# Performance work log

Measured on AMD Instinct MI355X. Metric: run time of the kernel, lower is better.

## Reference

```python
import jax, jax.numpy as jnp
import numpy as np

N_NODES = 100000


def setup_inputs() -> dict:
    key = jax.random.key(0)
    ks = jax.random.split(key, 7)
    n, d, c, e = N_NODES, 256, 128, 3200000
    features = jax.random.normal(ks[0], (n, d), dtype=jnp.float32)
    adj_row = jax.random.randint(ks[1], (e,), 0, n, dtype=jnp.int32)
    adj_col = jax.random.randint(ks[2], (e,), 0, n, dtype=jnp.int32)
    adj_vals = jax.random.uniform(ks[3], (e,), dtype=jnp.float32)
    kernel = jax.random.normal(ks[4], (d, c), dtype=jnp.float32) * (1.0 / np.sqrt(d))
    bias = jax.random.normal(ks[5], (c,), dtype=jnp.float32) * 0.01
    skip_weight = jax.random.normal(ks[6], (c,), dtype=jnp.float32)
    return {"features": features, "adj_row": adj_row, "adj_col": adj_col,
            "adj_vals": adj_vals, "kernel": kernel, "bias": bias,
            "skip_weight": skip_weight}


def reference(features, adj_row, adj_col, adj_vals, kernel, bias, skip_weight):
    # h = X @ W  : [n, c]
    h = features @ kernel
    # SpMM: out[r] += A[r, c] * h[c] over edges (COO)
    msgs = adj_vals[:, None] * h[adj_col]            # [e, c]
    agg = jax.ops.segment_sum(msgs, adj_row, num_segments=N_NODES)  # [n, c]
    out = h * skip_weight + agg                      # skip-connection scale + aggregation
    out = out + bias
    return jax.nn.selu(out)
```

## Files before the change

kernel.cpp:

```cpp
#include <hip/hip_runtime.h>
#include <math.h>

#define N_NODES 100000
#define D 256
#define C 128
#define N_EDGES 3200000

#define BROWS 128
#define NBUCKET ((N_NODES + BROWS - 1) / BROWS)
#define CAP 4608
#define EPB 8192
#define PBLOCKS ((N_EDGES + EPB - 1) / EPB)
#define NCH 13
#define NKEY (BROWS * NCH)

typedef __attribute__((ext_vector_type(8))) short bf16x8;
typedef __attribute__((ext_vector_type(4))) float f32x4;

__device__ __forceinline__ unsigned short f2bf(float f) {
  const unsigned int u = __float_as_uint(f);
  return (unsigned short)((u + 0x7fffu + ((u >> 16) & 1u)) >> 16);
}
__device__ __forceinline__ unsigned int pack_bf(float lo, float hi) {
  return (unsigned int)f2bf(lo) | ((unsigned int)f2bf(hi) << 16);
}
__device__ __forceinline__ float bflo(unsigned int u) {
  return __uint_as_float(u << 16);
}
__device__ __forceinline__ float bfhi(unsigned int u) {
  return __uint_as_float(u & 0xffff0000u);
}
__device__ __forceinline__ float selu1(float x) {
  const float scale = 1.0507009873554804934193349852946f;
  const float alpha = 1.6732632423543772848170429916717f;
  return x > 0.f ? scale * x : scale * alpha * (__expf(x) - 1.f);
}
__device__ __forceinline__ unsigned int pack_rec(int col, float val) {
  return ((unsigned int)col << 15) | ((unsigned int)f2bf(val) & 0x7fffu);
}
__device__ __forceinline__ float rec_val(unsigned int r) {
  return __uint_as_float((r & 0x7fffu) << 16);
}
__device__ __forceinline__ bf16x8 packA_nt(const float* p) {
  const f32x4 a0 = __builtin_nontemporal_load(reinterpret_cast<const f32x4*>(p));
  const f32x4 a1 =
      __builtin_nontemporal_load(reinterpret_cast<const f32x4*>(p) + 1);
  union {
    unsigned int u[4];
    bf16x8 v;
  } af;
  af.u[0] = pack_bf(a0[0], a0[1]);
  af.u[1] = pack_bf(a0[2], a0[3]);
  af.u[2] = pack_bf(a1[0], a1[1]);
  af.u[3] = pack_bf(a1[2], a1[3]);
  return af.v;
}

__global__ __launch_bounds__(256) void prep(const float* __restrict__ W,
                                            unsigned short* __restrict__ WT) {
  const int t = blockIdx.x * blockDim.x + threadIdx.x;
  const int n = t >> 8;
  const int k = t & 255;
  WT[t] = f2bf(W[k * C + n]);
}

__global__ __launch_bounds__(512) void gemm_partition(
    const float* __restrict__ X, const unsigned short* __restrict__ WT,
    unsigned short* __restrict__ h2, const int* __restrict__ row,
    const int* __restrict__ col, const float* __restrict__ vals,
    unsigned int* __restrict__ meta, uint2* __restrict__ recs) {
  __shared__ int hist[NBUCKET];
  __shared__ int scanA[1024];
  __shared__ int scanB[1024];
  const int bid = blockIdx.x;
  const int tid = threadIdx.x;

  if ((bid & 1) == 0) {
    const int wid = (bid >> 1) * 8 + (tid >> 6);
    const int row0 = wid * 32;
    if (row0 >= N_NODES) return;
    const int lane = tid & 63;
    const int r = lane & 15;
    const int kg = lane >> 4;

    f32x4 acc[2][8];
#pragma unroll
    for (int g = 0; g < 2; ++g)
#pragma unroll
      for (int f = 0; f < 8; ++f) acc[g][f] = (f32x4){0.f, 0.f, 0.f, 0.f};

    const float* arow0 = X + (size_t)(row0 + r) * D + kg * 8;
    const float* arow1 = arow0 + 16 * D;
    for (int k0 = 0; k0 < D; k0 += 32) {
      const bf16x8 a0 = packA_nt(arow0 + k0);
      const bf16x8 a1 = packA_nt(arow1 + k0);
#pragma unroll
      for (int f = 0; f < 8; ++f) {
        const bf16x8 bf = *reinterpret_cast<const bf16x8*>(
            WT + (size_t)(f * 16 + r) * D + k0 + kg * 8);
        acc[0][f] =
            __builtin_amdgcn_mfma_f32_16x16x32_bf16(a0, bf, acc[0][f], 0, 0, 0);
        acc[1][f] =
            __builtin_amdgcn_mfma_f32_16x16x32_bf16(a1, bf, acc[1][f], 0, 0, 0);
      }
    }
#pragma unroll
    for (int g = 0; g < 2; ++g)
#pragma unroll
      for (int f = 0; f < 8; ++f)
#pragma unroll
        for (int j = 0; j < 4; ++j)
          h2[(size_t)(row0 + g * 16 + kg * 4 + j) * C + f * 16 + r] =
              f2bf(acc[g][f][j]);
  } else {
    const int pb = bid >> 1;
    const int e0 = pb * EPB;
    for (int i = tid; i < NBUCKET; i += 512) hist[i] = 0;
    __syncthreads();

    unsigned int stash[16];
#pragma unroll
    for (int k = 0; k < 16; ++k) {
      const int e = e0 + k * 512 + tid;
      unsigned int s = 0xFFFFFFFFu;
      if (e < N_EDGES) {
        const int r = __builtin_nontemporal_load(row + e);
        const int off = atomicAdd(&hist[r >> 7], 1);
        s = (unsigned int)r | ((unsigned int)off << 17);
      }
      stash[k] = s;
    }
    __syncthreads();

    for (int i = tid; i < 1024; i += 512) scanA[i] = (i < NBUCKET) ? hist[i] : 0;
    __syncthreads();
    int* src = scanA;
    int* dst = scanB;
    for (int off = 1; off < 1024; off <<= 1) {
      for (int i = tid; i < 1024; i += 512)
        dst[i] = src[i] + ((i >= off) ? src[i - off] : 0);
      __syncthreads();
      int* tp = src;
      src = dst;
      dst = tp;
    }
    for (int b = tid; b < NBUCKET; b += 512) {
      const int sb = src[b] - hist[b];
      dst[b] = sb;
      meta[(size_t)pb * NBUCKET + b] =
          ((unsigned int)sb << 16) | (unsigned int)hist[b];
    }
    __syncthreads();

#pragma unroll
    for (int k = 0; k < 16; ++k) {
      const unsigned int s = stash[k];
      if (s == 0xFFFFFFFFu) continue;
      const int r = (int)(s & 0x1FFFFu);
      const int off = (int)(s >> 17);
      const int e = e0 + k * 512 + tid;
      const int c = __builtin_nontemporal_load(col + e);
      const float v = __builtin_nontemporal_load(vals + e);
      const int b = r >> 7;
      recs[(size_t)pb * EPB + dst[b] + off] =
          make_uint2(pack_rec(c, v), r & (BROWS - 1));
    }
  }
}

__global__ __launch_bounds__(512) void sort_gather_selu(
    const unsigned int* __restrict__ meta, const uint2* __restrict__ recs,
    const unsigned int* __restrict__ h2u, const float* __restrict__ skip,
    const float* __restrict__ bias, float* __restrict__ out) {
  __shared__ unsigned int sorted[CAP];
  __shared__ int hist[NKEY];
  __shared__ int start[2048];
  __shared__ int segA[512];
  __shared__ int segB[512];
  __shared__ unsigned int segglob[PBLOCKS];
  const int tid = threadIdx.x;
  const int b = blockIdx.x;

  int cnt = 0;
  if (tid < PBLOCKS) {
    const unsigned int m = meta[(size_t)tid * NBUCKET + b];
    cnt = (int)(m & 0xFFFFu);
    segglob[tid] = (unsigned int)tid * EPB + (m >> 16);
  }
  segA[tid] = cnt;
  for (int i = tid; i < NKEY; i += 512) hist[i] = 0;
  __syncthreads();
  int* s1 = segA;
  int* s2 = segB;
  for (int off = 1; off < 512; off <<= 1) {
    s2[tid] = s1[tid] + ((tid >= off) ? s1[tid - off] : 0);
    __syncthreads();
    int* tp = s1;
    s1 = s2;
    s2 = tp;
  }
  const int fill0 = s1[PBLOCKS - 1];
  const int fill = fill0 < CAP ? fill0 : CAP;

  uint2 stash[9];
  int nst = 0;
  for (int i = tid; i < fill; i += 512) {
    int lo = 0, hi = PBLOCKS - 1;
    while (lo < hi) {
      const int mid = (lo + hi) >> 1;
      if (s1[mid] > i) hi = mid;
      else lo = mid + 1;
    }
    const int idx = i - (lo ? s1[lo - 1] : 0);
    const unsigned long long rc = __builtin_nontemporal_load(
        reinterpret_cast<const unsigned long long*>(recs) + segglob[lo] + idx);
    const unsigned int cv = (unsigned int)rc;
    const unsigned int lr = (unsigned int)(rc >> 32);
    const unsigned int key = lr * NCH + (cv >> 28);
    const int off = atomicAdd(&hist[key], 1);
    stash[nst] = make_uint2(cv, key | ((unsigned int)off << 11));
    ++nst;
  }
  __syncthreads();

  for (int i = tid; i < 2048; i += 512) start[i] = (i < NKEY) ? hist[i] : 0;
  __syncthreads();
  for (int off = 1; off < 2048; off <<= 1) {
    int t[4];
#pragma unroll
    for (int q = 0; q < 4; ++q) {
      const int idx = tid + q * 512;
      t[q] = (idx >= off) ? start[idx - off] : 0;
    }
    __syncthreads();
#pragma unroll
    for (int q = 0; q < 4; ++q) start[tid + q * 512] += t[q];
    __syncthreads();
  }

  for (int k = 0; k < nst; ++k) {
    const int key = (int)(stash[k].y & 2047u);
    const int off = (int)(stash[k].y >> 11);
    sorted[start[key] - hist[key] + off] = stash[k].x;
  }
  __syncthreads();

  const int lane = tid & 63;
  const int wv = tid >> 6;
  for (int lr = wv; lr < BROWS; lr += 8) {
    const int grow = b * BROWS + lr;
    if (grow >= N_NODES) break;
    const int k0 = lr * NCH;
    const int je = start[k0 + NCH - 1];
    int j = start[k0] - hist[k0];
    float ax = 0.f, ay = 0.f;
    for (; j + 7 < je; j += 8) {
      unsigned int cc[8], uu[8];
#pragma unroll
      for (int q = 0; q < 8; ++q) cc[q] = sorted[j + q];
#pragma unroll
      for (int q = 0; q < 8; ++q) uu[q] = h2u[(size_t)(cc[q] >> 15) * 64 + lane];
#pragma unroll
      for (int q = 0; q < 8; ++q) {
        ax = fmaf(rec_val(cc[q]), bflo(uu[q]), ax);
        ay = fmaf(rec_val(cc[q]), bfhi(uu[q]), ay);
      }
    }
    for (; j + 3 < je; j += 4) {
      unsigned int cc[4], uu[4];
#pragma unroll
      for (int q = 0; q < 4; ++q) cc[q] = sorted[j + q];
#pragma unroll
      for (int q = 0; q < 4; ++q) uu[q] = h2u[(size_t)(cc[q] >> 15) * 64 + lane];
#pragma unroll
      for (int q = 0; q < 4; ++q) {
        ax = fmaf(rec_val(cc[q]), bflo(uu[q]), ax);
        ay = fmaf(rec_val(cc[q]), bfhi(uu[q]), ay);
      }
    }
    for (; j < je; ++j) {
      const unsigned int cc = sorted[j];
      const unsigned int u = h2u[(size_t)(cc >> 15) * 64 + lane];
      ax = fmaf(rec_val(cc), bflo(u), ax);
      ay = fmaf(rec_val(cc), bfhi(u), ay);
    }
    const unsigned int hr = h2u[(size_t)grow * 64 + lane];
    const float2 sk = *reinterpret_cast<const float2*>(skip + lane * 2);
    const float2 bi = *reinterpret_cast<const float2*>(bias + lane * 2);
    const float ox = selu1(fmaf(bflo(hr), sk.x, ax) + bi.x);
    const float oy = selu1(fmaf(bfhi(hr), sk.y, ay) + bi.y);
    *reinterpret_cast<float2*>(out + (size_t)grow * C + lane * 2) =
        make_float2(ox, oy);
  }
}

extern "C" void kernel_launch(void* const* d_in, const int* in_sizes, int n_in,
                              void* d_out, int out_size, void* d_ws,
                              size_t ws_size, hipStream_t stream) {
  const float* features = (const float*)d_in[0];
  const int* adj_row = (const int*)d_in[1];
  const int* adj_col = (const int*)d_in[2];
  const float* adj_vals = (const float*)d_in[3];
  const float* W = (const float*)d_in[4];
  const float* bias = (const float*)d_in[5];
  const float* skip = (const float*)d_in[6];
  float* out = (float*)d_out;

  char* ws = (char*)d_ws;
  const size_t SZ_H2 = (size_t)N_NODES * C * 2;
  const size_t OFF_RECS = (SZ_H2 + 255) & ~(size_t)255;
  const size_t SZ_RECS = (size_t)PBLOCKS * EPB * 8;
  const size_t OFF_META = OFF_RECS + SZ_RECS;
  const size_t SZ_META = (size_t)PBLOCKS * NBUCKET * 4;
  const size_t OFF_WT = (OFF_META + SZ_META + 255) & ~(size_t)255;
  const size_t NEEDED = OFF_WT + (size_t)D * C * 2;

  if (ws_size < NEEDED) return;

  unsigned short* h2 = (unsigned short*)ws;
  uint2* recs = (uint2*)(ws + OFF_RECS);
  unsigned int* meta = (unsigned int*)(ws + OFF_META);
  unsigned short* WT = (unsigned short*)(ws + OFF_WT);

  prep<<<(D * C) / 256, 256, 0, stream>>>(W, WT);

  gemm_partition<<<2 * PBLOCKS, 512, 0, stream>>>(
      features, WT, h2, adj_row, adj_col, adj_vals, meta, recs);

  sort_gather_selu<<<NBUCKET, 512, 0, stream>>>(
      meta, recs, (const unsigned int*)h2, skip, bias, out);
}
```

Baseline: 285.8 us.

## Gather SpMM by column chunk across all rows of a bucket for cache locality

The aggregation loop is reordered so each wave keeps 16 per-row accumulators in registers and walks the column chunks in the outer loop, visiting every row's edges in chunk c before moving to chunk c+1. All waves then gather h rows from the same column range at the same time, which is meant to improve L2/cache hit rates for the random h gathers. In exchange, register use rises from the 32 accumulators, the 8-wide unroll is dropped for a 4-wide one, and the per-row loop overhead grows with the extra chunk segments.

Result: slower. 318.5 us (+11.4%).

```diff
diff --git a/kernel.cpp b/kernel.cpp
--- a/kernel.cpp
+++ b/kernel.cpp
@@ -247,48 +247,53 @@
 
   const int lane = tid & 63;
   const int wv = tid >> 6;
-  for (int lr = wv; lr < BROWS; lr += 8) {
-    const int grow = b * BROWS + lr;
-    if (grow >= N_NODES) break;
-    const int k0 = lr * NCH;
-    const int je = start[k0 + NCH - 1];
-    int j = start[k0] - hist[k0];
-    float ax = 0.f, ay = 0.f;
-    for (; j + 7 < je; j += 8) {
-      unsigned int cc[8], uu[8];
-#pragma unroll
-      for (int q = 0; q < 8; ++q) cc[q] = sorted[j + q];
-#pragma unroll
-      for (int q = 0; q < 8; ++q) uu[q] = h2u[(size_t)(cc[q] >> 15) * 64 + lane];
-#pragma unroll
-      for (int q = 0; q < 8; ++q) {
-        ax = fmaf(rec_val(cc[q]), bflo(uu[q]), ax);
-        ay = fmaf(rec_val(cc[q]), bfhi(uu[q]), ay);
+  float ax[16], ay[16];
+#pragma unroll
+  for (int t = 0; t < 16; ++t) {
+    ax[t] = 0.f;
+    ay[t] = 0.f;
+  }
+  for (int c = 0; c < NCH; ++c) {
+#pragma unroll
+    for (int t = 0; t < 16; ++t) {
+      const int lr = wv + t * 8;
+      const int key = lr * NCH + c;
+      const int je = start[key];
+      int j = je - hist[key];
+      float sx = ax[t], sy = ay[t];
+      for (; j + 3 < je; j += 4) {
+        unsigned int cc[4], uu[4];
+#pragma unroll
+        for (int q = 0; q < 4; ++q) cc[q] = sorted[j + q];
+#pragma unroll
+        for (int q = 0; q < 4; ++q)
+          uu[q] = h2u[(size_t)(cc[q] >> 15) * 64 + lane];
+#pragma unroll
+        for (int q = 0; q < 4; ++q) {
+          sx = fmaf(rec_val(cc[q]), bflo(uu[q]), sx);
+          sy = fmaf(rec_val(cc[q]), bfhi(uu[q]), sy);
+        }
       }
-    }
-    for (; j + 3 < je; j += 4) {
-      unsigned int cc[4], uu[4];
-#pragma unroll
-      for (int q = 0; q < 4; ++q) cc[q] = sorted[j + q];
-#pragma unroll
-      for (int q = 0; q < 4; ++q) uu[q] = h2u[(size_t)(cc[q] >> 15) * 64 + lane];
-#pragma unroll
-      for (int q = 0; q < 4; ++q) {
-        ax = fmaf(rec_val(cc[q]), bflo(uu[q]), ax);
-        ay = fmaf(rec_val(cc[q]), bfhi(uu[q]), ay);
+      for (; j < je; ++j) {
+        const unsigned int cc = sorted[j];
+        const unsigned int u = h2u[(size_t)(cc >> 15) * 64 + lane];
+        sx = fmaf(rec_val(cc), bflo(u), sx);
+        sy = fmaf(rec_val(cc), bfhi(u), sy);
       }
-    }
-    for (; j < je; ++j) {
-      const unsigned int cc = sorted[j];
-      const unsigned int u = h2u[(size_t)(cc >> 15) * 64 + lane];
-      ax = fmaf(rec_val(cc), bflo(u), ax);
-      ay = fmaf(rec_val(cc), bfhi(u), ay);
-    }
+      ax[t] = sx;
+      ay[t] = sy;
+    }
+  }
+
+  const float2 sk = *reinterpret_cast<const float2*>(skip + lane * 2);
+  const float2 bi = *reinterpret_cast<const float2*>(bias + lane * 2);
+#pragma unroll
+  for (int t = 0; t < 16; ++t) {
+    const int grow = b * BROWS + wv + t * 8;
+    if (grow >= N_NODES) continue;
     const unsigned int hr = h2u[(size_t)grow * 64 + lane];
-    const float2 sk = *reinterpret_cast<const float2*>(skip + lane * 2);
-    const float2 bi = *reinterpret_cast<const float2*>(bias + lane * 2);
-    const float ox = selu1(fmaf(bflo(hr), sk.x, ax) + bi.x);
-    const float oy = selu1(fmaf(bfhi(hr), sk.y, ay) + bi.y);
+    const float ox = selu1(fmaf(bflo(hr), sk.x, ax[t]) + bi.x);
+    const float oy = selu1(fmaf(bfhi(hr), sk.y, ay[t]) + bi.y);
     *reinterpret_cast<float2*>(out + (size_t)grow * C + lane * 2) =
         make_float2(ox, oy);
   }
```

## Stage X tiles through LDS with coalesced loads and retile GEMM blocks

Applied to the files above, without the earlier changes.

The GEMM half of the fused gemm/partition kernel now loads 128-row tiles of X with coalesced float4 reads, converts them to bf16 and stages them in padded shared memory before the MFMA loop, replacing per-lane strided nontemporal loads straight into registers. Each wave handles 16 rows instead of 32, and the grid becomes 3 blocks per partition block (two GEMM, one partition) to cover all rows. This aims to improve global-load coalescing of the 100MB feature read. In exchange it adds LDS usage, which may reduce occupancy for the partition blocks, plus extra barriers.

After: 267.8 us (median of 2 runs). 6.3% less time.

```diff
diff --git a/kernel.cpp b/kernel.cpp
--- a/kernel.cpp
+++ b/kernel.cpp
@@ -14,6 +14,11 @@
 #define NCH 13
 #define NKEY (BROWS * NCH)
 
+#define GROWS 128
+#define NGB ((N_NODES + GROWS - 1) / GROWS)
+#define KH 128
+#define XPAD 136
+
 typedef __attribute__((ext_vector_type(8))) short bf16x8;
 typedef __attribute__((ext_vector_type(4))) float f32x4;
 
@@ -40,20 +45,6 @@
 }
 __device__ __forceinline__ float rec_val(unsigned int r) {
   return __uint_as_float((r & 0x7fffu) << 16);
-}
-__device__ __forceinline__ bf16x8 packA_nt(const float* p) {
-  const f32x4 a0 = __builtin_nontemporal_load(reinterpret_cast<const f32x4*>(p));
-  const f32x4 a1 =
-      __builtin_nontemporal_load(reinterpret_cast<const f32x4*>(p) + 1);
-  union {
-    unsigned int u[4];
-    bf16x8 v;
-  } af;
-  af.u[0] = pack_bf(a0[0], a0[1]);
-  af.u[1] = pack_bf(a0[2], a0[3]);
-  af.u[2] = pack_bf(a1[0], a1[1]);
-  af.u[3] = pack_bf(a1[2], a1[3]);
-  return af.v;
 }
 
 __global__ __launch_bounds__(256) void prep(const float* __restrict__ W,
@@ -69,51 +60,65 @@
     unsigned short* __restrict__ h2, const int* __restrict__ row,
     const int* __restrict__ col, const float* __restrict__ vals,
     unsigned int* __restrict__ meta, uint2* __restrict__ recs) {
+  __shared__ unsigned short xs[GROWS][XPAD];
   __shared__ int hist[NBUCKET];
   __shared__ int scanA[1024];
   __shared__ int scanB[1024];
   const int bid = blockIdx.x;
   const int tid = threadIdx.x;
-
-  if ((bid & 1) == 0) {
-    const int wid = (bid >> 1) * 8 + (tid >> 6);
-    const int row0 = wid * 32;
-    if (row0 >= N_NODES) return;
+  const int rem = bid % 3;
+
+  if (rem != 2) {
+    const int gid = (bid / 3) * 2 + rem;
+    const int rows0 = gid * GROWS;
     const int lane = tid & 63;
+    const int w = tid >> 6;
     const int r = lane & 15;
     const int kg = lane >> 4;
 
-    f32x4 acc[2][8];
-#pragma unroll
-    for (int g = 0; g < 2; ++g)
-#pragma unroll
-      for (int f = 0; f < 8; ++f) acc[g][f] = (f32x4){0.f, 0.f, 0.f, 0.f};
-
-    const float* arow0 = X + (size_t)(row0 + r) * D + kg * 8;
-    const float* arow1 = arow0 + 16 * D;
-    for (int k0 = 0; k0 < D; k0 += 32) {
-      const bf16x8 a0 = packA_nt(arow0 + k0);
-      const bf16x8 a1 = packA_nt(arow1 + k0);
-#pragma unroll
-      for (int f = 0; f < 8; ++f) {
-        const bf16x8 bf = *reinterpret_cast<const bf16x8*>(
-            WT + (size_t)(f * 16 + r) * D + k0 + kg * 8);
-        acc[0][f] =
-            __builtin_amdgcn_mfma_f32_16x16x32_bf16(a0, bf, acc[0][f], 0, 0, 0);
-        acc[1][f] =
-            __builtin_amdgcn_mfma_f32_16x16x32_bf16(a1, bf, acc[1][f], 0, 0, 0);
-      }
-    }
-#pragma unroll
-    for (int g = 0; g < 2; ++g)
-#pragma unroll
-      for (int f = 0; f < 8; ++f)
-#pragma unroll
-        for (int j = 0; j < 4; ++j)
-          h2[(size_t)(row0 + g * 16 + kg * 4 + j) * C + f * 16 + r] =
-              f2bf(acc[g][f][j]);
+    f32x4 acc[8];
+#pragma unroll
+    for (int f = 0; f < 8; ++f) acc[f] = (f32x4){0.f, 0.f, 0.f, 0.f};
+
+#pragma unroll
+    for (int h = 0; h < 2; ++h) {
+#pragma unroll
+      for (int i = 0; i < 8; ++i) {
+        const int lrow = w * 16 + i * 2 + (lane >> 5);
+        const int grow = rows0 + lrow;
+        const int kc = (lane & 31) * 4;
+        f32x4 x = (f32x4){0.f, 0.f, 0.f, 0.f};
+        if (grow < N_NODES)
+          x = *reinterpret_cast<const f32x4*>(X + (size_t)grow * D + h * KH +
+                                              kc);
+        const unsigned int p0 = pack_bf(x[0], x[1]);
+        const unsigned int p1 = pack_bf(x[2], x[3]);
+        *reinterpret_cast<uint2*>(&xs[lrow][kc]) = make_uint2(p0, p1);
+      }
+      __syncthreads();
+#pragma unroll
+      for (int ks = 0; ks < 4; ++ks) {
+        const bf16x8 a =
+            *reinterpret_cast<const bf16x8*>(&xs[w * 16 + r][ks * 32 + kg * 8]);
+#pragma unroll
+        for (int f = 0; f < 8; ++f) {
+          const bf16x8 bf = *reinterpret_cast<const bf16x8*>(
+              WT + (size_t)(f * 16 + r) * D + h * KH + ks * 32 + kg * 8);
+          acc[f] =
+              __builtin_amdgcn_mfma_f32_16x16x32_bf16(a, bf, acc[f], 0, 0, 0);
+        }
+      }
+      __syncthreads();
+    }
+#pragma unroll
+    for (int f = 0; f < 8; ++f)
+#pragma unroll
+      for (int j = 0; j < 4; ++j) {
+        const int grow = rows0 + w * 16 + kg * 4 + j;
+        if (grow < N_NODES) h2[(size_t)grow * C + f * 16 + r] = f2bf(acc[f][j]);
+      }
   } else {
-    const int pb = bid >> 1;
+    const int pb = bid / 3;
     const int e0 = pb * EPB;
     for (int i = tid; i < NBUCKET; i += 512) hist[i] = 0;
     __syncthreads();
@@ -324,7 +329,7 @@
 
   prep<<<(D * C) / 256, 256, 0, stream>>>(W, WT);
 
-  gemm_partition<<<2 * PBLOCKS, 512, 0, stream>>>(
+  gemm_partition<<<3 * PBLOCKS, 512, 0, stream>>>(
       features, WT, h2, adj_row, adj_col, adj_vals, meta, recs);
 
   sort_gather_selu<<<NBUCKET, 512, 0, stream>>>(
```
